# Performance work log

Measured on AMD Instinct MI355X. Metric: run time of the kernel, lower is better.

## Reference

```python
import jax, jax.numpy as jnp
import numpy as np

T, B, OBS, H, P, L, A = 512, 128, 512, 256, 128, 4, 4


def _ln(x, scale, bias, eps=1e-6):
    mu = jnp.mean(x, axis=-1, keepdims=True)
    var = jnp.mean((x - mu) ** 2, axis=-1, keepdims=True)
    return (x - mu) * jax.lax.rsqrt(var + eps) * scale + bias


def _binop(qi, qj):
    # S5 reset-aware associative operator: elements (A, b, reset_flag)
    Ai, bi, ci = qi
    Aj, bj, cj = qj
    A = (Aj * Ai) * (1.0 - cj) + Aj * cj
    b = (Aj * bi + bj) * (1.0 - cj) + bj * cj
    c = ci * (1.0 - cj) + cj
    return A, b, c


def _s5_layer(x, dones, h0, scale, bias, lam_re, lam_im, b_re, b_im, c_re, c_im, d_vec, log_step, glu_W, glu_b):
    # x: (T,B,H) real, dones: (T,B), h0: (B,P) complex64
    skip = x
    u = _ln(x, scale, bias)                                  # prenorm
    lam = lam_re + 1j * lam_im                               # (P,)
    step = jnp.exp(log_step)                                 # (P,)
    lam_bar = jnp.exp(lam * step)                            # ZOH discretization
    B_bar = ((lam_bar - 1.0) / lam)[:, None] * (b_re + 1j * b_im)  # (P,H)
    Bu = jnp.einsum('tbh,ph->tbp', u.astype(jnp.complex64), B_bar)  # (T,B,P)
    A_el = jnp.concatenate([jnp.ones((1, B, P), jnp.complex64),
                            jnp.broadcast_to(lam_bar.astype(jnp.complex64), (T, B, P))], axis=0)
    b_el = jnp.concatenate([h0[None], Bu], axis=0)
    c_el = jnp.concatenate([jnp.zeros((1, B, 1), jnp.float32), dones[..., None]], axis=0)
    _, xs, _ = jax.lax.associative_scan(_binop, (A_el, b_el, c_el), axis=0)
    xs = xs[1:]                                              # (T,B,P) complex states
    new_h = xs[-1]
    C = c_re + 1j * c_im                                     # (H,P)
    ys = 2.0 * jnp.real(jnp.einsum('tbp,hp->tbh', xs, C)) + d_vec * u  # conj_sym output + D*u
    z = _ln(ys, scale, bias)                                 # gtrxl norm (shared LayerNorm params)
    z = jax.nn.gelu(z)                                       # half_glu1
    z = z * jax.nn.sigmoid(z @ glu_W + glu_b)
    return skip + z, new_h


def setup_inputs() -> dict:
    key = jax.random.key(0)
    ks = jax.random.split(key, 40)
    f32 = jnp.float32

    def n(i, shape, s=1.0):
        return jax.random.normal(ks[i], shape, f32) * s

    inp = {}
    inp['obs'] = n(0, (T, B, OBS))
    inp['dones'] = (jax.random.uniform(ks[1], (T, B)) < 0.01).astype(f32)
    inp['hidden_re'] = jnp.zeros((L, B, P), f32)
    inp['hidden_im'] = jnp.zeros((L, B, P), f32)
    inp['enc0_W'] = n(2, (OBS, 128), 1.0 / np.sqrt(OBS))
    inp['enc0_b'] = jnp.zeros((128,), f32)
    inp['enc1_W'] = n(3, (128, H), 1.0 / np.sqrt(128))
    inp['enc1_b'] = jnp.zeros((H,), f32)
    inp['norm_scale'] = jnp.ones((L, H), f32)
    inp['norm_bias'] = jnp.zeros((L, H), f32)
    inp['Lambda_re'] = -0.5 * jax.random.uniform(ks[4], (L, P), f32) - 0.1
    inp['Lambda_im'] = n(5, (L, P), np.pi)
    inp['B_re'] = n(6, (L, P, H), 1.0 / np.sqrt(H))
    inp['B_im'] = n(7, (L, P, H), 1.0 / np.sqrt(H))
    inp['C_re'] = n(8, (L, H, P), 1.0 / np.sqrt(2 * P))
    inp['C_im'] = n(9, (L, H, P), 1.0 / np.sqrt(2 * P))
    inp['D'] = n(10, (L, H))
    inp['log_step'] = jax.random.uniform(ks[11], (L, P), f32, np.log(1e-3), np.log(1e-1))
    inp['glu_W'] = n(12, (L, H, H), 1.0 / np.sqrt(H))
    inp['glu_b'] = jnp.zeros((L, H), f32)
    inp['ab0_W'] = n(13, (H, 128), 1.0 / np.sqrt(H))
    inp['ab0_b'] = jnp.zeros((128,), f32)
    inp['ab1_W'] = n(14, (128, 128), 1.0 / np.sqrt(128))
    inp['ab1_b'] = jnp.zeros((128,), f32)
    inp['adec_W'] = n(15, (128, A), 0.01 / np.sqrt(128))
    inp['adec_b'] = jnp.full((A,), 0.5, f32)
    inp['log_std'] = jnp.full((A,), -0.7, f32)
    inp['vb0_W'] = n(16, (H, 128), 1.0 / np.sqrt(H))
    inp['vb0_b'] = jnp.zeros((128,), f32)
    inp['vb1_W'] = n(17, (128, 128), 1.0 / np.sqrt(128))
    inp['vb1_b'] = jnp.zeros((128,), f32)
    inp['vdec_W'] = n(18, (128, 1), 1.0 / np.sqrt(128))
    inp['vdec_b'] = jnp.zeros((1,), f32)
    return inp


def reference(obs, dones, hidden_re, hidden_im, enc0_W, enc0_b, enc1_W, enc1_b,
              norm_scale, norm_bias, Lambda_re, Lambda_im, B_re, B_im, C_re, C_im,
              D, log_step, glu_W, glu_b, ab0_W, ab0_b, ab1_W, ab1_b, adec_W, adec_b,
              log_std, vb0_W, vb0_b, vb1_W, vb1_b, vdec_W, vdec_b):
    e = jax.nn.leaky_relu(obs @ enc0_W + enc0_b)
    e = jax.nn.leaky_relu(e @ enc1_W + enc1_b)
    h0 = (hidden_re + 1j * hidden_im).astype(jnp.complex64)  # (L,B,P)
    new_h = []
    for l in range(L):
        e, hl = _s5_layer(e, dones, h0[l], norm_scale[l], norm_bias[l],
                          Lambda_re[l], Lambda_im[l], B_re[l], B_im[l],
                          C_re[l], C_im[l], D[l], log_step[l], glu_W[l], glu_b[l])
        new_h.append(hl)
    new_h = jnp.stack(new_h)
    am = jax.nn.leaky_relu(e @ ab0_W + ab0_b)
    am = jax.nn.leaky_relu(am @ ab1_W + ab1_b)
    am = am @ adec_W + adec_b                                # actor mean (T,B,A)
    v = jax.nn.leaky_relu(e @ vb0_W + vb0_b)
    v = jax.nn.leaky_relu(v @ vb1_W + vb1_b)
    v = v @ vdec_W + vdec_b                                  # critic (T,B,1)
    sc = jnp.broadcast_to(jnp.exp(log_std), am.shape)        # Normal scale (pi params)
    out = jnp.concatenate([am, sc, v], axis=-1)              # (T,B,2A+1)
    return out, jnp.real(new_h), jnp.imag(new_h)
```

## Files before the change

### kernel.cpp

```cpp
#include <hip/hip_runtime.h>
#include <math.h>

#define TT 512
#define BB 128
#define OBSD 512
#define HD 256
#define PD 128
#define LD 4
#define NTB (TT*BB)

typedef __bf16 bf16x8 __attribute__((ext_vector_type(8)));
typedef float  f32x4  __attribute__((ext_vector_type(4)));

__device__ __forceinline__ float bf2f(unsigned short u) {
    return __uint_as_float(((unsigned)u) << 16);
}
__device__ __forceinline__ unsigned short f2bf(float f) {
    unsigned u = __float_as_uint(f);
    unsigned r = (u + 0x7FFFu + ((u >> 16) & 1u)) >> 16;
    return (unsigned short)r;
}
__device__ __forceinline__ float gelu_f(float x) {
    float x3 = x * x * x;
    return 0.5f * x * (1.f + tanhf(0.7978845608028654f * (x + 0.044715f * x3)));
}

template<int MODE, int NJ>
__global__ __launch_bounds__(256) void mgemm2(
    const unsigned short* __restrict__ A, const unsigned short* __restrict__ BT,
    int K, const float* __restrict__ bias,
    const float* __restrict__ lnsc, const float* __restrict__ lnbi,
    const unsigned short* __restrict__ aux1, unsigned short* Xio,
    unsigned short* __restrict__ U, int wU)
{
    const int N = NJ * 64;
    __shared__ unsigned short smA[2][64 * 32];
    __shared__ unsigned short smB[2][NJ * 64 * 32];
    float2 (*red)[4] = reinterpret_cast<float2(*)[4]>(&smA[0][0]);
    int tid = threadIdx.x;
    int lane = tid & 63, w = tid >> 6;
    int m16 = lane & 15, quad = lane >> 4;
    int m0 = blockIdx.x * 64;

    f32x4 acc[4][NJ] = {};

    auto stage = [&](int bu, int k0) {
        const unsigned short* g = A + (size_t)(m0 + (tid >> 2)) * K + k0 + (tid & 3) * 8;
        __builtin_amdgcn_global_load_lds(
            (const __attribute__((address_space(1))) void*)g,
            (__attribute__((address_space(3))) void*)(&smA[bu][0] + tid * 8), 16, 0, 0);
#pragma unroll
        for (int p = 0; p < NJ; ++p) {
            const unsigned short* gb = BT + (size_t)(p * 64 + (tid >> 2)) * K + k0 + (tid & 3) * 8;
            __builtin_amdgcn_global_load_lds(
                (const __attribute__((address_space(1))) void*)gb,
                (__attribute__((address_space(3))) void*)(&smB[bu][0] + p * 2048 + tid * 8), 16, 0, 0);
        }
    };

    int nk = K >> 5;
    stage(0, 0);
    for (int t = 0; t < nk; ++t) {
        int cur = t & 1;
        if (t + 1 < nk) {
            stage(cur ^ 1, (t + 1) << 5);
            asm volatile("s_waitcnt vmcnt(%0)" :: "i"(NJ + 1) : "memory");
        } else {
            asm volatile("s_waitcnt vmcnt(0)" ::: "memory");
        }
        __builtin_amdgcn_s_barrier();
        __builtin_amdgcn_sched_barrier(0);
        bf16x8 af[4], bfr[NJ];
#pragma unroll
        for (int mi = 0; mi < 4; ++mi)
            af[mi] = *(const bf16x8*)(&smA[cur][0] + (mi * 16 + m16) * 32 + quad * 8);
#pragma unroll
        for (int nj = 0; nj < NJ; ++nj)
            bfr[nj] = *(const bf16x8*)(&smB[cur][0] + (w * NJ * 16 + nj * 16 + m16) * 32 + quad * 8);
#pragma unroll
        for (int mi = 0; mi < 4; ++mi)
#pragma unroll
            for (int nj = 0; nj < NJ; ++nj)
                acc[mi][nj] = __builtin_amdgcn_mfma_f32_16x16x32_bf16(
                    bfr[nj], af[mi], acc[mi][nj], 0, 0, 0);
        __builtin_amdgcn_sched_barrier(0);
        __builtin_amdgcn_s_barrier();
    }

    int colb = w * NJ * 16 + quad * 4;

    if (MODE == 1) {
#pragma unroll
        for (int mi = 0; mi < 4; ++mi) {
            size_t rowb = (size_t)(m0 + mi * 16 + m16) * N;
#pragma unroll
            for (int nj = 0; nj < NJ; ++nj) {
                ushort4 o = { f2bf(acc[mi][nj][0]), f2bf(acc[mi][nj][1]),
                              f2bf(acc[mi][nj][2]), f2bf(acc[mi][nj][3]) };
                *(ushort4*)(U + rowb + colb + nj * 16) = o;
            }
        }
        return;
    }

    float4 bn[NJ];
#pragma unroll
    for (int nj = 0; nj < NJ; ++nj) bn[nj] = *(const float4*)(bias + colb + nj * 16);

#pragma unroll
    for (int mi = 0; mi < 4; ++mi) {
        size_t rowb = (size_t)(m0 + mi * 16 + m16) * N;
        float s = 0.f, q = 0.f;
#pragma unroll
        for (int nj = 0; nj < NJ; ++nj) {
            ushort4 a1, xo;
            if (MODE == 2 || MODE == 3) a1 = *(const ushort4*)(aux1 + rowb + colb + nj * 16);
            if (MODE == 3)              xo = *(const ushort4*)(Xio + rowb + colb + nj * 16);
            float vv[4];
#pragma unroll
            for (int r = 0; r < 4; ++r) {
                float v = acc[mi][nj][r];
                float bv = (r == 0) ? bn[nj].x : (r == 1) ? bn[nj].y : (r == 2) ? bn[nj].z : bn[nj].w;
                if (MODE == 0 || MODE == 4) {
                    v += bv; v = v > 0.f ? v : 0.01f * v;
                } else if (MODE == 2) {
                    float u = bf2f(r == 0 ? a1.x : r == 1 ? a1.y : r == 2 ? a1.z : a1.w);
                    v += bv * u;
                } else if (MODE == 3) {
                    float zz = bf2f(r == 0 ? a1.x : r == 1 ? a1.y : r == 2 ? a1.z : a1.w);
                    float xx = bf2f(r == 0 ? xo.x : r == 1 ? xo.y : r == 2 ? xo.z : xo.w);
                    float sg = 1.f / (1.f + expf(-(v + bv)));
                    v = xx + zz * sg;
                }
                vv[r] = v;
                acc[mi][nj][r] = v;
                s += v; q += v * v;
            }
            if (MODE == 0 || MODE == 3) {
                ushort4 o = { f2bf(vv[0]), f2bf(vv[1]), f2bf(vv[2]), f2bf(vv[3]) };
                *(ushort4*)(Xio + rowb + colb + nj * 16) = o;
            } else if (MODE == 4) {
                ushort4 o = { f2bf(vv[0]), f2bf(vv[1]), f2bf(vv[2]), f2bf(vv[3]) };
                *(ushort4*)(U + rowb + colb + nj * 16) = o;
            }
        }
        if (MODE != 4 && (MODE != 3 || wU)) {
            s += __shfl_xor(s, 16); q += __shfl_xor(q, 16);
            s += __shfl_xor(s, 32); q += __shfl_xor(q, 32);
            if (quad == 0) red[mi * 16 + m16][w] = float2{s, q};
        }
    }
    if (MODE == 4 || (MODE == 3 && !wU)) return;
    __syncthreads();

    float4 ls[NJ], lb[NJ];
#pragma unroll
    for (int nj = 0; nj < NJ; ++nj) {
        ls[nj] = *(const float4*)(lnsc + colb + nj * 16);
        lb[nj] = *(const float4*)(lnbi + colb + nj * 16);
    }
#pragma unroll
    for (int mi = 0; mi < 4; ++mi) {
        int row_l = mi * 16 + m16;
        float2 t0 = red[row_l][0], t1 = red[row_l][1], t2 = red[row_l][2], t3 = red[row_l][3];
        float S = t0.x + t1.x + t2.x + t3.x;
        float Q = t0.y + t1.y + t2.y + t3.y;
        float mu = S * (1.f / 256.f);
        float var = Q * (1.f / 256.f) - mu * mu;
        float rstd = rsqrtf(var + 1e-6f);
        size_t rowb = (size_t)(m0 + row_l) * N;
#pragma unroll
        for (int nj = 0; nj < NJ; ++nj) {
            float o[4];
#pragma unroll
            for (int r = 0; r < 4; ++r) {
                float sc = (r == 0) ? ls[nj].x : (r == 1) ? ls[nj].y : (r == 2) ? ls[nj].z : ls[nj].w;
                float bi = (r == 0) ? lb[nj].x : (r == 1) ? lb[nj].y : (r == 2) ? lb[nj].z : lb[nj].w;
                float v = (acc[mi][nj][r] - mu) * rstd * sc + bi;
                if (MODE == 2) v = gelu_f(v);
                o[r] = v;
            }
            ushort4 ov = { f2bf(o[0]), f2bf(o[1]), f2bf(o[2]), f2bf(o[3]) };
            *(ushort4*)(U + rowb + colb + nj * 16) = ov;
        }
    }
}

__global__ __launch_bounds__(256) void mgemm_obs(
    const float* __restrict__ A, const unsigned short* __restrict__ BT,
    unsigned short* __restrict__ U, const float* __restrict__ bias)
{
    const int K = 512, NJ = 2, N = 128;
    __shared__ unsigned short smA[64 * 32];
    __shared__ unsigned short smB[NJ * 64 * 32];
    int tid = threadIdx.x;
    int lane = tid & 63, w = tid >> 6;
    int m16 = lane & 15, quad = lane >> 4;
    int m0 = blockIdx.x * 64;

    f32x4 acc[4][NJ] = {};
    for (int k0 = 0; k0 < K; k0 += 32) {
#pragma unroll
        for (int p = 0; p < 2; ++p) {
            int idx = p * 256 + tid;
            int r = idx >> 3, kq = (idx & 7) * 4;
            float4 v = *(const float4*)(A + (size_t)(m0 + r) * K + k0 + kq);
            ushort4 o = { f2bf(v.x), f2bf(v.y), f2bf(v.z), f2bf(v.w) };
            *(ushort4*)(smA + r * 32 + kq) = o;
        }
#pragma unroll
        for (int p = 0; p < NJ; ++p) {
            const unsigned short* g = BT + (size_t)(p * 64 + (tid >> 2)) * K + k0 + (tid & 3) * 8;
            unsigned short* l = smB + p * 2048 + tid * 8;
            __builtin_amdgcn_global_load_lds(
                (const __attribute__((address_space(1))) void*)g,
                (__attribute__((address_space(3))) void*)l, 16, 0, 0);
        }
        __syncthreads();
        bf16x8 af[4], bfr[NJ];
#pragma unroll
        for (int mi = 0; mi < 4; ++mi)
            af[mi] = *(const bf16x8*)(smA + (mi * 16 + m16) * 32 + quad * 8);
#pragma unroll
        for (int nj = 0; nj < NJ; ++nj)
            bfr[nj] = *(const bf16x8*)(smB + (w * NJ * 16 + nj * 16 + m16) * 32 + quad * 8);
#pragma unroll
        for (int mi = 0; mi < 4; ++mi)
#pragma unroll
            for (int nj = 0; nj < NJ; ++nj)
                acc[mi][nj] = __builtin_amdgcn_mfma_f32_16x16x32_bf16(
                    bfr[nj], af[mi], acc[mi][nj], 0, 0, 0);
        __syncthreads();
    }
    int colb = w * NJ * 16 + quad * 4;
#pragma unroll
    for (int mi = 0; mi < 4; ++mi) {
        size_t rowb = (size_t)(m0 + mi * 16 + m16) * N;
#pragma unroll
        for (int nj = 0; nj < NJ; ++nj) {
            float4 bv = *(const float4*)(bias + colb + nj * 16);
            float v0 = acc[mi][nj][0] + bv.x; v0 = v0 > 0.f ? v0 : 0.01f * v0;
            float v1 = acc[mi][nj][1] + bv.y; v1 = v1 > 0.f ? v1 : 0.01f * v1;
            float v2 = acc[mi][nj][2] + bv.z; v2 = v2 > 0.f ? v2 : 0.01f * v2;
            float v3 = acc[mi][nj][3] + bv.w; v3 = v3 > 0.f ? v3 : 0.01f * v3;
            ushort4 o = { f2bf(v0), f2bf(v1), f2bf(v2), f2bf(v3) };
            *(ushort4*)(U + rowb + colb + nj * 16) = o;
        }
    }
}

__global__ __launch_bounds__(512) void scan2_k(
    const unsigned short* __restrict__ bu, unsigned short* __restrict__ xs,
    const float* __restrict__ dones,
    const float* __restrict__ h0re, const float* __restrict__ h0im,
    const float* __restrict__ lamre, const float* __restrict__ lamim,
    const float* __restrict__ lstep,
    float* __restrict__ outre, float* __restrict__ outim)
{
    __shared__ float sdone[TT];
    __shared__ float4 ssum[8][64];
    __shared__ float2 shin[8][64];
    int tid = threadIdx.x;
    int b  = blockIdx.x >> 1;
    int ph = blockIdx.x & 1;
    int chunk = tid >> 6, pl = tid & 63;
    int p = ph * 64 + pl;
    sdone[tid] = dones[tid * BB + b];
    float lr = lamre[p], li = lamim[p];
    float st = expf(lstep[p]);
    float er = expf(lr * st);
    float ar = er * cosf(li * st);
    float ai = er * sinf(li * st);
    __syncthreads();

    int t0 = chunk * 64;
    unsigned buf[64];
    float Ar = 1.f, Ai = 0.f, br = 0.f, bi = 0.f;
#pragma unroll
    for (int j = 0; j < 64; ++j) {
        size_t off = ((size_t)(t0 + j) * BB + b) * 256 + 2 * p;
        unsigned v = *(const unsigned*)(bu + off);
        buf[j] = v;
        float bur = bf2f((unsigned short)(v & 0xFFFFu));
        float bui = bf2f((unsigned short)(v >> 16));
        if (sdone[t0 + j] != 0.f) {
            Ar = 0.f; Ai = 0.f; br = bur; bi = bui;
        } else {
            float nAr = ar * Ar - ai * Ai;
            float nAi = ar * Ai + ai * Ar;
            float nbr = fmaf(ar, br, fmaf(-ai, bi, bur));
            float nbi = fmaf(ar, bi, fmaf(ai, br, bui));
            Ar = nAr; Ai = nAi; br = nbr; bi = nbi;
        }
    }
    ssum[chunk][pl] = float4{Ar, Ai, br, bi};
    __syncthreads();
    if (tid < 64) {
        int gid = b * 128 + p;
        float hr = h0re[gid], hi = h0im[gid];
#pragma unroll
        for (int c = 0; c < 8; ++c) {
            shin[c][pl] = float2{hr, hi};
            float4 s = ssum[c][pl];
            float nhr = fmaf(s.x, hr, fmaf(-s.y, hi, s.z));
            float nhi = fmaf(s.x, hi, fmaf(s.y, hr, s.w));
            hr = nhr; hi = nhi;
        }
        outre[gid] = hr; outim[gid] = hi;
    }
    __syncthreads();
    float hr = shin[chunk][pl].x, hi = shin[chunk][pl].y;
#pragma unroll
    for (int j = 0; j < 64; ++j) {
        unsigned v = buf[j];
        float bur = bf2f((unsigned short)(v & 0xFFFFu));
        float bui = bf2f((unsigned short)(v >> 16));
        float nr, ni;
        if (sdone[t0 + j] != 0.f) { nr = bur; ni = bui; }
        else {
            nr = fmaf(ar, hr, fmaf(-ai, hi, bur));
            ni = fmaf(ar, hi, fmaf(ai, hr, bui));
        }
        hr = nr; hi = ni;
        size_t off = ((size_t)(t0 + j) * BB + b) * 256 + 2 * p;
        *(unsigned*)(xs + off) = ((unsigned)f2bf(ni) << 16) | f2bf(nr);
    }
}

__global__ __launch_bounds__(256) void prep_k(
    const float* __restrict__ Br, const float* __restrict__ Bi,
    const float* __restrict__ Cr, const float* __restrict__ Ci,
    const float* __restrict__ Lr, const float* __restrict__ Li,
    const float* __restrict__ ls, unsigned short* bbarT, unsigned short* ccatT)
{
    int gid = blockIdx.x * 256 + threadIdx.x;
    int l = gid >> 15;
    int rem = gid & 32767;
    int p = rem >> 8;
    int h = rem & 255;
    float lr = Lr[l * PD + p], li = Li[l * PD + p];
    float st = expf(ls[l * PD + p]);
    float er = expf(lr * st);
    float lbr = er * cosf(li * st);
    float lbi = er * sinf(li * st);
    float nr = lbr - 1.f, ni = lbi;
    float den = lr * lr + li * li;
    float fr = (nr * lr + ni * li) / den;
    float fi = (ni * lr - nr * li) / den;
    float bre = Br[(size_t)(l * PD + p) * HD + h];
    float bim = Bi[(size_t)(l * PD + p) * HD + h];
    size_t lb = (size_t)l * 65536;
    bbarT[lb + (size_t)(2 * p) * 256 + h]     = f2bf(fr * bre - fi * bim);
    bbarT[lb + (size_t)(2 * p + 1) * 256 + h] = f2bf(fr * bim + fi * bre);
    float cre = Cr[(size_t)(l * HD + h) * PD + p];
    float cim = Ci[(size_t)(l * HD + h) * PD + p];
    ccatT[lb + (size_t)h * 256 + 2 * p]     = f2bf(2.f * cre);
    ccatT[lb + (size_t)h * 256 + 2 * p + 1] = f2bf(-2.f * cim);
}

__global__ __launch_bounds__(256) void tcvt_k(const float* __restrict__ in,
    unsigned short* __restrict__ out, int K, int N)
{
    int gid = blockIdx.x * 256 + threadIdx.x;
    if (gid >= K * N) return;
    int k = gid / N, n = gid - k * N;
    out[(size_t)n * K + k] = f2bf(in[gid]);
}

__global__ __launch_bounds__(256) void tcvt4_k(const float* __restrict__ in,
    unsigned short* __restrict__ out)
{
    int gid = blockIdx.x * 256 + threadIdx.x;
    int l = gid >> 16;
    int rem = gid & 65535;
    int k = rem >> 8, n = rem & 255;
    out[(size_t)l * 65536 + (size_t)n * 256 + k] = f2bf(in[gid]);
}

__global__ __launch_bounds__(256) void head_k(
    const unsigned short* __restrict__ am2, const unsigned short* __restrict__ v2,
    const float* __restrict__ adW, const float* __restrict__ adb,
    const float* __restrict__ lstd,
    const float* __restrict__ vdW, const float* __restrict__ vdb,
    float* out)
{
    int wid = threadIdx.x >> 6, lane = threadIdx.x & 63;
    size_t row = (size_t)blockIdx.x * 4 + wid;
    float a1 = bf2f(am2[row * 128 + lane]);
    float a2 = bf2f(am2[row * 128 + 64 + lane]);
    float w1 = bf2f(v2[row * 128 + lane]);
    float w2 = bf2f(v2[row * 128 + 64 + lane]);
    float vals[5];
#pragma unroll
    for (int a = 0; a < 4; ++a)
        vals[a] = a1 * adW[lane * 4 + a] + a2 * adW[(lane + 64) * 4 + a];
    vals[4] = w1 * vdW[lane] + w2 * vdW[64 + lane];
#pragma unroll
    for (int off = 32; off; off >>= 1)
#pragma unroll
        for (int k = 0; k < 5; ++k) vals[k] += __shfl_xor(vals[k], off);
    if (lane == 0) {
        size_t o = row * 9;
#pragma unroll
        for (int a = 0; a < 4; ++a) out[o + a] = vals[a] + adb[a];
#pragma unroll
        for (int a = 0; a < 4; ++a) out[o + 4 + a] = expf(lstd[a]);
        out[o + 8] = vals[4] + vdb[0];
    }
}

extern "C" void kernel_launch(void* const* d_in, const int* in_sizes, int n_in,
                              void* d_out, int out_size, void* d_ws, size_t ws_size,
                              hipStream_t stream) {
    (void)in_sizes; (void)n_in; (void)out_size; (void)ws_size;
    const float* obs     = (const float*)d_in[0];
    const float* dones   = (const float*)d_in[1];
    const float* hre     = (const float*)d_in[2];
    const float* him     = (const float*)d_in[3];
    const float* enc0_W  = (const float*)d_in[4];
    const float* enc0_b  = (const float*)d_in[5];
    const float* enc1_W  = (const float*)d_in[6];
    const float* enc1_b  = (const float*)d_in[7];
    const float* nsc     = (const float*)d_in[8];
    const float* nbi     = (const float*)d_in[9];
    const float* Lre     = (const float*)d_in[10];
    const float* Lim     = (const float*)d_in[11];
    const float* B_re    = (const float*)d_in[12];
    const float* B_im    = (const float*)d_in[13];
    const float* C_re    = (const float*)d_in[14];
    const float* C_im    = (const float*)d_in[15];
    const float* Dv      = (const float*)d_in[16];
    const float* lstep   = (const float*)d_in[17];
    const float* glu_W   = (const float*)d_in[18];
    const float* glu_b   = (const float*)d_in[19];
    const float* ab0_W   = (const float*)d_in[20];
    const float* ab0_b   = (const float*)d_in[21];
    const float* ab1_W   = (const float*)d_in[22];
    const float* ab1_b   = (const float*)d_in[23];
    const float* adec_W  = (const float*)d_in[24];
    const float* adec_b  = (const float*)d_in[25];
    const float* log_std = (const float*)d_in[26];
    const float* vb0_W   = (const float*)d_in[27];
    const float* vb0_b   = (const float*)d_in[28];
    const float* vb1_W   = (const float*)d_in[29];
    const float* vb1_b   = (const float*)d_in[30];
    const float* vdec_W  = (const float*)d_in[31];
    const float* vdec_b  = (const float*)d_in[32];

    const size_t MB = (size_t)1 << 20;
    char* wsb = (char*)d_ws;
    unsigned short* XS    = (unsigned short*)(wsb);
    unsigned short* AM1   = (unsigned short*)(wsb);
    unsigned short* V1    = (unsigned short*)(wsb + 16 * MB);
    unsigned short* AM2   = (unsigned short*)(wsb + 32 * MB);
    unsigned short* V2    = (unsigned short*)(wsb + 48 * MB);
    unsigned short* U1    = (unsigned short*)(wsb + 64 * MB);
    unsigned short* X     = (unsigned short*)(wsb + 96 * MB);
    unsigned short* U     = (unsigned short*)(wsb + 128 * MB);
    unsigned short* BU    = (unsigned short*)(wsb + 160 * MB);
    char* wgt = wsb + 192 * MB;
    unsigned short* BBART = (unsigned short*)(wgt);
    unsigned short* CCATT = (unsigned short*)(wgt + 512 * 1024);
    unsigned short* GLUT  = (unsigned short*)(wgt + 1024 * 1024);
    unsigned short* E0T   = (unsigned short*)(wgt + 1536 * 1024);
    unsigned short* E1T   = (unsigned short*)(wgt + 1664 * 1024);
    unsigned short* AB0T  = (unsigned short*)(wgt + 1728 * 1024);
    unsigned short* AB1T  = (unsigned short*)(wgt + 1792 * 1024);
    unsigned short* VB0T  = (unsigned short*)(wgt + 1824 * 1024);
    unsigned short* VB1T  = (unsigned short*)(wgt + 1888 * 1024);

    float* out   = (float*)d_out;
    float* outre = out + (size_t)NTB * 9;
    float* outim = outre + LD * BB * PD;

    prep_k<<<512, 256, 0, stream>>>(B_re, B_im, C_re, C_im, Lre, Lim, lstep, BBART, CCATT);
    tcvt_k<<<256, 256, 0, stream>>>(enc0_W, E0T, 512, 128);
    tcvt_k<<<128, 256, 0, stream>>>(enc1_W, E1T, 128, 256);
    tcvt4_k<<<1024, 256, 0, stream>>>(glu_W, GLUT);
    tcvt_k<<<128, 256, 0, stream>>>(ab0_W, AB0T, 256, 128);
    tcvt_k<<<64, 256, 0, stream>>>(ab1_W, AB1T, 128, 128);
    tcvt_k<<<128, 256, 0, stream>>>(vb0_W, VB0T, 256, 128);
    tcvt_k<<<64, 256, 0, stream>>>(vb1_W, VB1T, 128, 128);

    mgemm_obs<<<1024, 256, 0, stream>>>(obs, E0T, U1, enc0_b);
    mgemm2<0, 4><<<1024, 256, 0, stream>>>(U1, E1T, 128, enc1_b, nsc, nbi, nullptr, X, U, 1);

    for (int l = 0; l < LD; ++l) {
        mgemm2<1, 4><<<1024, 256, 0, stream>>>(U, BBART + (size_t)l * 65536, 256,
                                               nullptr, nullptr, nullptr, nullptr, nullptr, BU, 0);
        scan2_k<<<256, 512, 0, stream>>>(BU, XS, dones, hre + l * BB * PD, him + l * BB * PD,
                                         Lre + l * PD, Lim + l * PD, lstep + l * PD,
                                         outre + l * BB * PD, outim + l * BB * PD);
        mgemm2<2, 4><<<1024, 256, 0, stream>>>(XS, CCATT + (size_t)l * 65536, 256,
                                               Dv + l * HD, nsc + l * HD, nbi + l * HD, U, nullptr, U, 1);
        const float* nsc2 = nsc + ((l + 1 < LD) ? (l + 1) * HD : 0);
        const float* nbi2 = nbi + ((l + 1 < LD) ? (l + 1) * HD : 0);
        mgemm2<3, 4><<<1024, 256, 0, stream>>>(U, GLUT + (size_t)l * 65536, 256,
                                               glu_b + l * HD, nsc2, nbi2, U, X, U, (l + 1 < LD) ? 1 : 0);
    }

    mgemm2<4, 2><<<1024, 256, 0, stream>>>(X, AB0T, 256, ab0_b, nullptr, nullptr, nullptr, nullptr, AM1, 0);
    mgemm2<4, 2><<<1024, 256, 0, stream>>>(AM1, AB1T, 128, ab1_b, nullptr, nullptr, nullptr, nullptr, AM2, 0);
    mgemm2<4, 2><<<1024, 256, 0, stream>>>(X, VB0T, 256, vb0_b, nullptr, nullptr, nullptr, nullptr, V1, 0);
    mgemm2<4, 2><<<1024, 256, 0, stream>>>(V1, VB1T, 128, vb1_b, nullptr, nullptr, nullptr, nullptr, V2, 0);
    head_k<<<NTB / 4, 256, 0, stream>>>(AM2, V2, adec_W, adec_b, log_std, vdec_W, vdec_b, out);
}
```

Baseline: 964.5 us.

## Fuse actor/critic first-layer GEMMs and add occupancy launch bounds

Concatenates the actor and critic first-layer weights and biases so a single N=256 GEMM reads X once instead of twice, and the second-layer GEMMs read their halves through a new leading-dimension parameter. It also adds min-blocks hints to the launch bounds of the GEMM kernels and moves bias/LayerNorm parameter loads into the inner loops, both meant to cut register pressure. This removes one GEMM launch and one full pass over X, at the cost of a strided A read in the second layers and possible spilling under the tighter register budget.

```diff
diff --git a/kernel.cpp b/kernel.cpp
--- a/kernel.cpp
+++ b/kernel.cpp
@@ -26,9 +26,9 @@
 }
 
 template<int MODE, int NJ>
-__global__ __launch_bounds__(256) void mgemm2(
+__global__ __launch_bounds__(256, 4) void mgemm2(
     const unsigned short* __restrict__ A, const unsigned short* __restrict__ BT,
-    int K, const float* __restrict__ bias,
+    int K, int LDA, const float* __restrict__ bias,
     const float* __restrict__ lnsc, const float* __restrict__ lnbi,
     const unsigned short* __restrict__ aux1, unsigned short* Xio,
     unsigned short* __restrict__ U, int wU)
@@ -45,7 +45,7 @@
     f32x4 acc[4][NJ] = {};
 
     auto stage = [&](int bu, int k0) {
-        const unsigned short* g = A + (size_t)(m0 + (tid >> 2)) * K + k0 + (tid & 3) * 8;
+        const unsigned short* g = A + (size_t)(m0 + (tid >> 2)) * LDA + k0 + (tid & 3) * 8;
         __builtin_amdgcn_global_load_lds(
             (const __attribute__((address_space(1))) void*)g,
             (__attribute__((address_space(3))) void*)(&smA[bu][0] + tid * 8), 16, 0, 0);
@@ -103,16 +103,13 @@
         return;
     }
 
-    float4 bn[NJ];
-#pragma unroll
-    for (int nj = 0; nj < NJ; ++nj) bn[nj] = *(const float4*)(bias + colb + nj * 16);
-
 #pragma unroll
     for (int mi = 0; mi < 4; ++mi) {
         size_t rowb = (size_t)(m0 + mi * 16 + m16) * N;
         float s = 0.f, q = 0.f;
 #pragma unroll
         for (int nj = 0; nj < NJ; ++nj) {
+            float4 bn = *(const float4*)(bias + colb + nj * 16);
             ushort4 a1, xo;
             if (MODE == 2 || MODE == 3) a1 = *(const ushort4*)(aux1 + rowb + colb + nj * 16);
             if (MODE == 3)              xo = *(const ushort4*)(Xio + rowb + colb + nj * 16);
@@ -120,7 +117,7 @@
 #pragma unroll
             for (int r = 0; r < 4; ++r) {
                 float v = acc[mi][nj][r];
-                float bv = (r == 0) ? bn[nj].x : (r == 1) ? bn[nj].y : (r == 2) ? bn[nj].z : bn[nj].w;
+                float bv = (r == 0) ? bn.x : (r == 1) ? bn.y : (r == 2) ? bn.z : bn.w;
                 if (MODE == 0 || MODE == 4) {
                     v += bv; v = v > 0.f ? v : 0.01f * v;
                 } else if (MODE == 2) {
@@ -153,12 +150,6 @@
     if (MODE == 4 || (MODE == 3 && !wU)) return;
     __syncthreads();
 
-    float4 ls[NJ], lb[NJ];
-#pragma unroll
-    for (int nj = 0; nj < NJ; ++nj) {
-        ls[nj] = *(const float4*)(lnsc + colb + nj * 16);
-        lb[nj] = *(const float4*)(lnbi + colb + nj * 16);
-    }
 #pragma unroll
     for (int mi = 0; mi < 4; ++mi) {
         int row_l = mi * 16 + m16;
@@ -171,11 +162,13 @@
         size_t rowb = (size_t)(m0 + row_l) * N;
 #pragma unroll
         for (int nj = 0; nj < NJ; ++nj) {
+            float4 ls = *(const float4*)(lnsc + colb + nj * 16);
+            float4 lb = *(const float4*)(lnbi + colb + nj * 16);
             float o[4];
 #pragma unroll
             for (int r = 0; r < 4; ++r) {
-                float sc = (r == 0) ? ls[nj].x : (r == 1) ? ls[nj].y : (r == 2) ? ls[nj].z : ls[nj].w;
-                float bi = (r == 0) ? lb[nj].x : (r == 1) ? lb[nj].y : (r == 2) ? lb[nj].z : lb[nj].w;
+                float sc = (r == 0) ? ls.x : (r == 1) ? ls.y : (r == 2) ? ls.z : ls.w;
+                float bi = (r == 0) ? lb.x : (r == 1) ? lb.y : (r == 2) ? lb.z : lb.w;
                 float v = (acc[mi][nj][r] - mu) * rstd * sc + bi;
                 if (MODE == 2) v = gelu_f(v);
                 o[r] = v;
@@ -186,7 +179,7 @@
     }
 }
 
-__global__ __launch_bounds__(256) void mgemm_obs(
+__global__ __launch_bounds__(256, 4) void mgemm_obs(
     const float* __restrict__ A, const unsigned short* __restrict__ BT,
     unsigned short* __restrict__ U, const float* __restrict__ bias)
 {
@@ -375,6 +368,13 @@
     int rem = gid & 65535;
     int k = rem >> 8, n = rem & 255;
     out[(size_t)l * 65536 + (size_t)n * 256 + k] = f2bf(in[gid]);
+}
+
+__global__ __launch_bounds__(256) void catb_k(const float* __restrict__ a,
+    const float* __restrict__ b, float* __restrict__ out)
+{
+    int i = threadIdx.x;
+    out[i] = (i < 128) ? a[i] : b[i - 128];
 }
 
 __global__ __launch_bounds__(256) void head_k(
@@ -450,8 +450,7 @@
     const size_t MB = (size_t)1 << 20;
     char* wsb = (char*)d_ws;
     unsigned short* XS    = (unsigned short*)(wsb);
-    unsigned short* AM1   = (unsigned short*)(wsb);
-    unsigned short* V1    = (unsigned short*)(wsb + 16 * MB);
+    unsigned short* AMV1  = (unsigned short*)(wsb);
     unsigned short* AM2   = (unsigned short*)(wsb + 32 * MB);
     unsigned short* V2    = (unsigned short*)(wsb + 48 * MB);
     unsigned short* U1    = (unsigned short*)(wsb + 64 * MB);
@@ -464,10 +463,10 @@
     unsigned short* GLUT  = (unsigned short*)(wgt + 1024 * 1024);
     unsigned short* E0T   = (unsigned short*)(wgt + 1536 * 1024);
     unsigned short* E1T   = (unsigned short*)(wgt + 1664 * 1024);
-    unsigned short* AB0T  = (unsigned short*)(wgt + 1728 * 1024);
-    unsigned short* AB1T  = (unsigned short*)(wgt + 1792 * 1024);
-    unsigned short* VB0T  = (unsigned short*)(wgt + 1824 * 1024);
+    unsigned short* AB0VT = (unsigned short*)(wgt + 1728 * 1024);
+    unsigned short* AB1T  = (unsigned short*)(wgt + 1856 * 1024);
     unsigned short* VB1T  = (unsigned short*)(wgt + 1888 * 1024);
+    float*          CB0   = (float*)(wgt + 1920 * 1024);
 
     float* out   = (float*)d_out;
     float* outre = out + (size_t)NTB * 9;
@@ -477,31 +476,31 @@
     tcvt_k<<<256, 256, 0, stream>>>(enc0_W, E0T, 512, 128);
     tcvt_k<<<128, 256, 0, stream>>>(enc1_W, E1T, 128, 256);
     tcvt4_k<<<1024, 256, 0, stream>>>(glu_W, GLUT);
-    tcvt_k<<<128, 256, 0, stream>>>(ab0_W, AB0T, 256, 128);
+    tcvt_k<<<128, 256, 0, stream>>>(ab0_W, AB0VT, 256, 128);
+    tcvt_k<<<128, 256, 0, stream>>>(vb0_W, AB0VT + 128 * 256, 256, 128);
     tcvt_k<<<64, 256, 0, stream>>>(ab1_W, AB1T, 128, 128);
-    tcvt_k<<<128, 256, 0, stream>>>(vb0_W, VB0T, 256, 128);
     tcvt_k<<<64, 256, 0, stream>>>(vb1_W, VB1T, 128, 128);
+    catb_k<<<1, 256, 0, stream>>>(ab0_b, vb0_b, CB0);
 
     mgemm_obs<<<1024, 256, 0, stream>>>(obs, E0T, U1, enc0_b);
-    mgemm2<0, 4><<<1024, 256, 0, stream>>>(U1, E1T, 128, enc1_b, nsc, nbi, nullptr, X, U, 1);
+    mgemm2<0, 4><<<1024, 256, 0, stream>>>(U1, E1T, 128, 128, enc1_b, nsc, nbi, nullptr, X, U, 1);
 
     for (int l = 0; l < LD; ++l) {
-        mgemm2<1, 4><<<1024, 256, 0, stream>>>(U, BBART + (size_t)l * 65536, 256,
+        mgemm2<1, 4><<<1024, 256, 0, stream>>>(U, BBART + (size_t)l * 65536, 256, 256,
                                                nullptr, nullptr, nullptr, nullptr, nullptr, BU, 0);
         scan2_k<<<256, 512, 0, stream>>>(BU, XS, dones, hre + l * BB * PD, him + l * BB * PD,
                                          Lre + l * PD, Lim + l * PD, lstep + l * PD,
                                          outre + l * BB * PD, outim + l * BB * PD);
-        mgemm2<2, 4><<<1024, 256, 0, stream>>>(XS, CCATT + (size_t)l * 65536, 256,
+        mgemm2<2, 4><<<1024, 256, 0, stream>>>(XS, CCATT + (size_t)l * 65536, 256, 256,
                                                Dv + l * HD, nsc + l * HD, nbi + l * HD, U, nullptr, U, 1);
         const float* nsc2 = nsc + ((l + 1 < LD) ? (l + 1) * HD : 0);
         const float* nbi2 = nbi + ((l + 1 < LD) ? (l + 1) * HD : 0);
-        mgemm2<3, 4><<<1024, 256, 0, stream>>>(U, GLUT + (size_t)l * 65536, 256,
+        mgemm2<3, 4><<<1024, 256, 0, stream>>>(U, GLUT + (size_t)l * 65536, 256, 256,
                                                glu_b + l * HD, nsc2, nbi2, U, X, U, (l + 1 < LD) ? 1 : 0);
     }
 
-    mgemm2<4, 2><<<1024, 256, 0, stream>>>(X, AB0T, 256, ab0_b, nullptr, nullptr, nullptr, nullptr, AM1, 0);
-    mgemm2<4, 2><<<1024, 256, 0, stream>>>(AM1, AB1T, 128, ab1_b, nullptr, nullptr, nullptr, nullptr, AM2, 0);
-    mgemm2<4, 2><<<1024, 256, 0, stream>>>(X, VB0T, 256, vb0_b, nullptr, nullptr, nullptr, nullptr, V1, 0);
-    mgemm2<4, 2><<<1024, 256, 0, stream>>>(V1, VB1T, 128, vb1_b, nullptr, nullptr, nullptr, nullptr, V2, 0);
+    mgemm2<4, 4><<<1024, 256, 0, stream>>>(X, AB0VT, 256, 256, CB0, nullptr, nullptr, nullptr, nullptr, AMV1, 0);
+    mgemm2<4, 2><<<1024, 256, 0, stream>>>(AMV1, AB1T, 128, 256, ab1_b, nullptr, nullptr, nullptr, nullptr, AM2, 0);
+    mgemm2<4, 2><<<1024, 256, 0, stream>>>(AMV1 + 128, VB1T, 128, 256, vb1_b, nullptr, nullptr, nullptr, nullptr, V2, 0);
     head_k<<<NTB / 4, 256, 0, stream>>>(AM2, V2, adec_W, adec_b, log_std, vdec_W, vdec_b, out);
 }
```

After: 1.048 ms. 8.7% more time.
